# Optimization experiments

Hardware: AMD Instinct MI355X
Metric: run time of the kernel (lower is better)

## Reference

```python
import jax, jax.numpy as jnp
import numpy as np

N, D, E = 16384, 256, 8
H = D // 2  # gate hidden


def setup_inputs() -> dict:
    key = jax.random.key(0)
    ks = jax.random.split(key, 10)
    s = lambda fan_in: 1.0 / np.sqrt(fan_in)
    return {
        "x":   jax.random.normal(ks[0], (N, D), dtype=jnp.float32),
        # gate: Linear(D, D//2) -> ReLU -> Linear(D//2, E) -> Softmax
        "Wg1": jax.random.uniform(ks[1], (D, H), jnp.float32, -s(D), s(D)),
        "bg1": jax.random.uniform(ks[2], (H,), jnp.float32, -s(D), s(D)),
        "Wg2": jax.random.uniform(ks[3], (H, E), jnp.float32, -s(H), s(H)),
        "bg2": jax.random.uniform(ks[4], (E,), jnp.float32, -s(H), s(H)),
        # experts: per-expert Linear(D,D) -> ReLU -> (Dropout eval=identity) -> Linear(D,D)
        "W1": jax.random.uniform(ks[5], (E, D, D), jnp.float32, -s(D), s(D)),
        "b1": jax.random.uniform(ks[6], (E, D), jnp.float32, -s(D), s(D)),
        "W2": jax.random.uniform(ks[7], (E, D, D), jnp.float32, -s(D), s(D)),
        "b2": jax.random.uniform(ks[8], (E, D), jnp.float32, -s(D), s(D)),
    }


def reference(x, Wg1, bg1, Wg2, bg2, W1, b1, W2, b2):
    # gate: [N, E] softmax over experts
    g = jax.nn.softmax(jax.nn.relu(x @ Wg1 + bg1) @ Wg2 + bg2, axis=-1)
    # all experts applied densely via batched GEMMs (fuses the Python loop)
    h = jax.nn.relu(jnp.einsum("nd,edh->neh", x, W1) + b1)  # [N, E, D]
    y = jnp.einsum("neh,ehd->ned", h, W2) + b2              # [N, E, D]
    # weighted combine: sum_e g[n,e] * y[n,e,:]
    return jnp.einsum("ned,ne->nd", y, g)
```

## Files before the change

### kernel.cpp

```cpp
#include <hip/hip_runtime.h>


typedef unsigned short USH;
typedef float f32x4 __attribute__((ext_vector_type(4)));
typedef __bf16 bf16x8 __attribute__((ext_vector_type(8)));

#define AS1 __attribute__((address_space(1)))
#define AS3 __attribute__((address_space(3)))

#define KS 2112

__device__ __forceinline__ USH f2bf(float f) {
  unsigned int u = __float_as_uint(f);
  u += 0x7fffu + ((u >> 16) & 1u);
  return (USH)(u >> 16);
}

__device__ __forceinline__ void gl2lds16(const void* g, void* l) {
  __builtin_amdgcn_global_load_lds((AS1 const void*)g, (AS3 void*)l, 16, 0, 0);
}


__global__ __launch_bounds__(256) void k_prep(
    const float* __restrict__ x,
    const float* __restrict__ Wg1,
    const float* __restrict__ W1,
    const float* __restrict__ W2,  const float* __restrict__ b2,
    USH* __restrict__ xb, USH* __restrict__ wg1t,
    USH* __restrict__ w1t, USH* __restrict__ w2t) {
  __shared__ float T[64][65];
  int b = blockIdx.x, tid = threadIdx.x;

  if (b < 2048) {
    size_t i8 = ((size_t)b * 256 + tid) * 8;
    float4 a = *(const float4*)(x + i8);
    float4 c = *(const float4*)(x + i8 + 4);
    USH v[8];
    v[0] = f2bf(a.x); v[1] = f2bf(a.y); v[2] = f2bf(a.z); v[3] = f2bf(a.w);
    v[4] = f2bf(c.x); v[5] = f2bf(c.y); v[6] = f2bf(c.z); v[7] = f2bf(c.w);
    *(uint4*)(xb + i8) = *(const uint4*)v;
  } else if (b < 2176) {
    int bp = b - 2048;
    int e = bp >> 4, tl = bp & 15;
    int c0 = (tl >> 2) * 64, h0 = (tl & 3) * 64;
    const float* src = W1 + (size_t)e * 65536;
#pragma unroll
    for (int p = 0; p < 4; ++p) {
      int r = p * 16 + (tid >> 4), d4 = (tid & 15) * 4;
      float4 v = *(const float4*)(src + (size_t)(c0 + r) * 256 + h0 + d4);
      T[r][d4] = v.x; T[r][d4 + 1] = v.y; T[r][d4 + 2] = v.z; T[r][d4 + 3] = v.w;
    }
    __syncthreads();
#pragma unroll
    for (int p = 0; p < 4; ++p) {
      int hr = p * 16 + (tid >> 4), c4 = (tid & 15) * 4;
      USH w[4];
#pragma unroll
      for (int j = 0; j < 4; ++j) w[j] = f2bf(T[c4 + j][hr]);
      *(uint2*)(w1t + (size_t)e * 65536 + (size_t)(h0 + hr) * 256 + c0 + c4) = *(const uint2*)w;
    }
  } else if (b < 2184) {
    int bp = b - 2176;
    int c0 = (bp >> 1) * 64, h0 = (bp & 1) * 64;
#pragma unroll
    for (int p = 0; p < 4; ++p) {
      int r = p * 16 + (tid >> 4), d4 = (tid & 15) * 4;
      float4 v = *(const float4*)(Wg1 + (size_t)(c0 + r) * 128 + h0 + d4);
      T[r][d4] = v.x; T[r][d4 + 1] = v.y; T[r][d4 + 2] = v.z; T[r][d4 + 3] = v.w;
    }
    __syncthreads();
#pragma unroll
    for (int p = 0; p < 4; ++p) {
      int hr = p * 16 + (tid >> 4), c4 = (tid & 15) * 4;
      USH w[4];
#pragma unroll
      for (int j = 0; j < 4; ++j) w[j] = f2bf(T[c4 + j][hr]);
      *(uint2*)(wg1t + (size_t)(h0 + hr) * 256 + c0 + c4) = *(const uint2*)w;
    }
  } else if (b < 2312) {
    int bp = b - 2184;
    int e = bp >> 4, tl = bp & 15;
    int h0 = (tl >> 2) * 64, d0 = (tl & 3) * 64;
    const float* src = W2 + (size_t)e * 65536;
#pragma unroll
    for (int p = 0; p < 4; ++p) {
      int r = p * 16 + (tid >> 4), d4 = (tid & 15) * 4;
      float4 v = *(const float4*)(src + (size_t)(h0 + r) * 256 + d0 + d4);
      T[r][d4] = v.x; T[r][d4 + 1] = v.y; T[r][d4 + 2] = v.z; T[r][d4 + 3] = v.w;
    }
    __syncthreads();
#pragma unroll
    for (int p = 0; p < 4; ++p) {
      int dr = p * 16 + (tid >> 4), h4 = (tid & 15) * 4;
      USH w[4];
#pragma unroll
      for (int j = 0; j < 4; ++j) w[j] = f2bf(T[h4 + j][dr]);
      *(uint2*)(w2t + (size_t)(d0 + dr) * KS + e * 256 + h0 + h4) = *(const uint2*)w;
    }
  } else {
    size_t base = (size_t)tid * KS + 2048;
#pragma unroll
    for (int p = 0; p < 16; ++p) {
      USH w[4];
#pragma unroll
      for (int j = 0; j < 4; ++j) {
        int e = p * 4 + j;
        w[j] = (e < 8) ? f2bf(b2[e * 256 + tid]) : (USH)0;
      }
      *(uint2*)(w2t + base + p * 4) = *(const uint2*)w;
    }
  }
}


__global__ __launch_bounds__(256) void k_gate(const USH* __restrict__ xb,
                                              const USH* __restrict__ wg1t,
                                              const float* __restrict__ bg1,
                                              const float* __restrict__ wg2,
                                              const float* __restrict__ bg2,
                                              float* __restrict__ g,
                                              USH* __restrict__ hw) {
  __shared__ __align__(16) USH As[32 * 64];
  __shared__ __align__(16) USH Bs[128 * 64];
  __shared__ float hg[32 * 129];
  __shared__ float bg1s[128];
  __shared__ float w2s[128 * 8];
  __shared__ float b2s[8];
  __shared__ float lg[32 * 8];

  int tid = threadIdx.x;
  int wave = tid >> 6, lane = tid & 63;
  int quad = lane >> 4, l16 = lane & 15;
  int sw = l16 & 7;
  int wr = wave >> 1, wc = wave & 1;
  int rowBase = blockIdx.x * 32;

  for (int t = tid; t < 1024; t += 256) w2s[t] = wg2[t];
  if (tid < 8) b2s[tid] = bg2[tid];
  if (tid < 128) bg1s[tid] = bg1[tid];

  f32x4 acc[4] = {};
  for (int kt = 0; kt < 4; ++kt) {
    int kb = kt * 64;
    {
      int r = tid >> 3, c8 = (tid & 7) ^ (r & 7);
      gl2lds16(xb + (size_t)(rowBase + r) * 256 + kb + c8 * 8, As + (size_t)tid * 8);
    }
#pragma unroll
    for (int c = 0; c < 4; ++c) {
      int i = c * 256 + tid;
      int r = i >> 3, c8 = (i & 7) ^ (r & 7);
      gl2lds16(wg1t + (size_t)r * 256 + kb + c8 * 8, Bs + (size_t)i * 8);
    }
    __syncthreads();
#pragma unroll
    for (int kkc = 0; kkc < 8; kkc += 4) {
      bf16x8 av = *(const bf16x8*)(As + (wr * 16 + l16) * 64 + (((kkc + quad) ^ sw) * 8));
#pragma unroll
      for (int j = 0; j < 4; ++j) {
        bf16x8 bv = *(const bf16x8*)(Bs + (wc * 64 + j * 16 + l16) * 64 + (((kkc + quad) ^ sw) * 8));
        acc[j] = __builtin_amdgcn_mfma_f32_16x16x32_bf16(av, bv, acc[j], 0, 0, 0);
      }
    }
    __syncthreads();
  }

#pragma unroll
  for (int j = 0; j < 4; ++j)
#pragma unroll
    for (int r = 0; r < 4; ++r) {
      int row = wr * 16 + quad * 4 + r;
      int col = wc * 64 + j * 16 + l16;
      hg[row * 129 + col] = fmaxf(acc[j][r] + bg1s[col], 0.0f);
    }
  __syncthreads();

  {
    int row = tid >> 3, p = tid & 7;
    float s = b2s[p];
    for (int k = 0; k < 128; ++k) s += hg[row * 129 + k] * w2s[k * 8 + p];
    lg[row * 8 + p] = s;
  }
  __syncthreads();

  if (tid < 32) {
    float l[8];
    float m = -1e30f;
#pragma unroll
    for (int e = 0; e < 8; ++e) { l[e] = lg[tid * 8 + e]; m = fmaxf(m, l[e]); }
    float s = 0.0f;
#pragma unroll
    for (int e = 0; e < 8; ++e) { l[e] = expf(l[e] - m); s += l[e]; }
    float inv = 1.0f / s;
    size_t grow = rowBase + tid;
#pragma unroll
    for (int e = 0; e < 8; ++e) {
      float ge = l[e] * inv;
      g[grow * 8 + e] = ge;
      hw[grow * KS + 2048 + e] = f2bf(ge);
    }
#pragma unroll
    for (int z = 0; z < 56; ++z) hw[grow * KS + 2056 + z] = 0;
  }
}


__global__ __launch_bounds__(256) void k_stage1(const USH* __restrict__ xb,
                                                const USH* __restrict__ w1t,
                                                const float* __restrict__ b1,
                                                const float* __restrict__ g,
                                                USH* __restrict__ hw) {
  __shared__ __align__(16) USH As[128 * 64];
  __shared__ __align__(16) USH Bs[128 * 64];
  __shared__ float gs[128];
  __shared__ float b1s[128];

  int tid = threadIdx.x;
  int wave = tid >> 6, lane = tid & 63;
  int quad = lane >> 4, l16 = lane & 15;
  int sw = l16 & 7;
  int wr = wave >> 1, wc = wave & 1;
  int rowBase = blockIdx.x * 128;
  int colBase = blockIdx.y * 128;
  int e = blockIdx.z;

  if (tid < 128) {
    gs[tid] = g[(size_t)(rowBase + tid) * 8 + e];
    b1s[tid] = b1[e * 256 + colBase + tid];
  }

  const USH* B = w1t + (size_t)e * 65536;

  f32x4 acc[4][4] = {};
  for (int kt = 0; kt < 4; ++kt) {
    int kb = kt * 64;
#pragma unroll
    for (int c = 0; c < 4; ++c) {
      int i = c * 256 + tid;
      int r = i >> 3, c8 = (i & 7) ^ (r & 7);
      gl2lds16(xb + (size_t)(rowBase + r) * 256 + kb + c8 * 8, As + (size_t)i * 8);
      gl2lds16(B + (size_t)(colBase + r) * 256 + kb + c8 * 8, Bs + (size_t)i * 8);
    }
    __syncthreads();
#pragma unroll
    for (int kkc = 0; kkc < 8; kkc += 4) {
      int cs = ((kkc + quad) ^ sw) * 8;
      bf16x8 av[4], bv[4];
#pragma unroll
      for (int i = 0; i < 4; ++i)
        av[i] = *(const bf16x8*)(As + (wr * 64 + i * 16 + l16) * 64 + cs);
#pragma unroll
      for (int j = 0; j < 4; ++j)
        bv[j] = *(const bf16x8*)(Bs + (wc * 64 + j * 16 + l16) * 64 + cs);
#pragma unroll
      for (int i = 0; i < 4; ++i)
#pragma unroll
        for (int j = 0; j < 4; ++j)
          acc[i][j] = __builtin_amdgcn_mfma_f32_16x16x32_bf16(av[i], bv[j], acc[i][j], 0, 0, 0);
    }
    __syncthreads();
  }

#pragma unroll
  for (int i = 0; i < 4; ++i) {
#pragma unroll
    for (int r = 0; r < 4; ++r) {
      int rl = wr * 64 + i * 16 + quad * 4 + r;
      float gg = gs[rl];
      size_t grow = (size_t)(rowBase + rl);
#pragma unroll
      for (int j = 0; j < 4; ++j) {
        int cl = wc * 64 + j * 16 + l16;
        float v = fmaxf(acc[i][j][r] + b1s[cl], 0.0f) * gg;
        hw[grow * KS + e * 256 + colBase + cl] = f2bf(v);
      }
    }
  }
}


__global__ __launch_bounds__(256) void k_stage2(const USH* __restrict__ hwm,
                                                const USH* __restrict__ w2t,
                                                float* __restrict__ out) {
  __shared__ __align__(16) USH As[64 * 64];
  __shared__ __align__(16) USH Bs[64 * 64];

  int tid = threadIdx.x;
  int wave = tid >> 6, lane = tid & 63;
  int quad = lane >> 4, l16 = lane & 15;
  int sw = l16 & 7;
  int rowBase = blockIdx.x * 64;
  int colBase = blockIdx.y * 64;

  f32x4 acc[4] = {};
  for (int kt = 0; kt < 33; ++kt) {
    int kb = kt * 64;
#pragma unroll
    for (int c = 0; c < 2; ++c) {
      int i = c * 256 + tid;
      int r = i >> 3, c8 = (i & 7) ^ (r & 7);
      gl2lds16(hwm + (size_t)(rowBase + r) * KS + kb + c8 * 8, As + (size_t)i * 8);
      gl2lds16(w2t + (size_t)(colBase + r) * KS + kb + c8 * 8, Bs + (size_t)i * 8);
    }
    __syncthreads();
#pragma unroll
    for (int kkc = 0; kkc < 8; kkc += 4) {
      int cs = ((kkc + quad) ^ sw) * 8;
      bf16x8 av = *(const bf16x8*)(As + (wave * 16 + l16) * 64 + cs);
#pragma unroll
      for (int j = 0; j < 4; ++j) {
        bf16x8 bv = *(const bf16x8*)(Bs + (j * 16 + l16) * 64 + cs);
        acc[j] = __builtin_amdgcn_mfma_f32_16x16x32_bf16(av, bv, acc[j], 0, 0, 0);
      }
    }
    __syncthreads();
  }

#pragma unroll
  for (int j = 0; j < 4; ++j)
#pragma unroll
    for (int r = 0; r < 4; ++r) {
      int row = wave * 16 + quad * 4 + r;
      out[(size_t)(rowBase + row) * 256 + colBase + j * 16 + l16] = acc[j][r];
    }
}


extern "C" void kernel_launch(void* const* d_in, const int* in_sizes, int n_in,
                              void* d_out, int out_size, void* d_ws, size_t ws_size,
                              hipStream_t stream) {
  const float* x   = (const float*)d_in[0];
  const float* Wg1 = (const float*)d_in[1];
  const float* bg1 = (const float*)d_in[2];
  const float* Wg2 = (const float*)d_in[3];
  const float* bg2 = (const float*)d_in[4];
  const float* W1  = (const float*)d_in[5];
  const float* b1  = (const float*)d_in[6];
  const float* W2  = (const float*)d_in[7];
  const float* b2  = (const float*)d_in[8];
  float* out = (float*)d_out;

  char* ws = (char*)d_ws;
  USH*   xb   = (USH*)(ws);
  USH*   w1t  = (USH*)(ws + 8388608);
  USH*   wg1t = (USH*)(ws + 9437184);
  USH*   w2t  = (USH*)(ws + 9502720);
  float* g    = (float*)(ws + 10584064);
  USH*   hw   = (USH*)(ws + 11108352);

  hipLaunchKernelGGL(k_prep, dim3(2313), dim3(256), 0, stream,
                     x, Wg1, W1, W2, b2, xb, wg1t, w1t, w2t);
  hipLaunchKernelGGL(k_gate,   dim3(512),       dim3(256), 0, stream, xb, wg1t, bg1, Wg2, bg2, g, hw);
  hipLaunchKernelGGL(k_stage1, dim3(128, 2, 8), dim3(256), 0, stream, xb, w1t, b1, g, hw);
  hipLaunchKernelGGL(k_stage2, dim3(256, 4),    dim3(256), 0, stream, hw, w2t, out);
}
```

Before: 148.1 us.

## Split-K stage2 into two halves with reduction kernel; stage stage1 epilogue through LDS

Stage2 now runs as a two-way split-K over the 33 K-tiles, writing partial sums to a workspace that a new elementwise kernel adds into the output. This doubles the number of blocks to fill the GPU better. Stage1's epilogue now stages the bf16 results through a swizzled LDS tile and writes them with 16-byte coalesced stores instead of scattered 2-byte stores. The split adds an extra 32 MB round trip of fp32 partials and one more kernel launch.

```diff
diff --git a/kernel.cpp b/kernel.cpp
--- a/kernel.cpp
+++ b/kernel.cpp
@@ -210,10 +210,11 @@
                                                 const float* __restrict__ b1,
                                                 const float* __restrict__ g,
                                                 USH* __restrict__ hw) {
-  __shared__ __align__(16) USH As[128 * 64];
-  __shared__ __align__(16) USH Bs[128 * 64];
+  __shared__ __align__(16) USH smem[128 * 64 * 2];
   __shared__ float gs[128];
   __shared__ float b1s[128];
+  USH* As = smem;
+  USH* Bs = smem + 128 * 64;
 
   int tid = threadIdx.x;
   int wave = tid >> 6, lane = tid & 63;
@@ -267,13 +268,25 @@
     for (int r = 0; r < 4; ++r) {
       int rl = wr * 64 + i * 16 + quad * 4 + r;
       float gg = gs[rl];
-      size_t grow = (size_t)(rowBase + rl);
 #pragma unroll
       for (int j = 0; j < 4; ++j) {
         int cl = wc * 64 + j * 16 + l16;
+        int q = (cl >> 3) ^ (quad << 1);
         float v = fmaxf(acc[i][j][r] + b1s[cl], 0.0f) * gg;
-        hw[grow * KS + e * 256 + colBase + cl] = f2bf(v);
+        smem[rl * 128 + q * 8 + (cl & 7)] = f2bf(v);
       }
+    }
+  }
+  __syncthreads();
+
+  {
+    int rr0 = tid >> 4, qrd = tid & 15;
+#pragma unroll
+    for (int pass = 0; pass < 8; ++pass) {
+      int rr = pass * 16 + rr0;
+      int qp = qrd ^ (((rr >> 2) & 3) << 1);
+      uint4 v = *(const uint4*)(smem + rr * 128 + qp * 8);
+      *(uint4*)(hw + (size_t)(rowBase + rr) * KS + e * 256 + colBase + qrd * 8) = v;
     }
   }
 }
@@ -281,7 +294,7 @@
 
 __global__ __launch_bounds__(256) void k_stage2(const USH* __restrict__ hwm,
                                                 const USH* __restrict__ w2t,
-                                                float* __restrict__ out) {
+                                                float* __restrict__ parts) {
   __shared__ __align__(16) USH As[64 * 64];
   __shared__ __align__(16) USH Bs[64 * 64];
 
@@ -291,9 +304,13 @@
   int sw = l16 & 7;
   int rowBase = blockIdx.x * 64;
   int colBase = blockIdx.y * 64;
+  int z = blockIdx.z;
+  int kt0 = z ? 17 : 0;
+  int kt1 = z ? 33 : 17;
+  float* out = parts + (size_t)z * 16384 * 256;
 
   f32x4 acc[4] = {};
-  for (int kt = 0; kt < 33; ++kt) {
+  for (int kt = kt0; kt < kt1; ++kt) {
     int kb = kt * 64;
 #pragma unroll
     for (int c = 0; c < 2; ++c) {
@@ -323,6 +340,17 @@
       int row = wave * 16 + quad * 4 + r;
       out[(size_t)(rowBase + row) * 256 + colBase + j * 16 + l16] = acc[j][r];
     }
+}
+
+
+__global__ __launch_bounds__(256) void k_add(const float* __restrict__ parts,
+                                             float* __restrict__ out) {
+  size_t i4 = ((size_t)blockIdx.x * 256 + threadIdx.x) * 4;
+  float4 a = *(const float4*)(parts + i4);
+  float4 b = *(const float4*)(parts + 4194304 + i4);
+  float4 o;
+  o.x = a.x + b.x; o.y = a.y + b.y; o.z = a.z + b.z; o.w = a.w + b.w;
+  *(float4*)(out + i4) = o;
 }
 
 
@@ -341,16 +369,18 @@
   float* out = (float*)d_out;
 
   char* ws = (char*)d_ws;
-  USH*   xb   = (USH*)(ws);
-  USH*   w1t  = (USH*)(ws + 8388608);
-  USH*   wg1t = (USH*)(ws + 9437184);
-  USH*   w2t  = (USH*)(ws + 9502720);
-  float* g    = (float*)(ws + 10584064);
-  USH*   hw   = (USH*)(ws + 11108352);
+  USH*   xb    = (USH*)(ws);
+  USH*   w1t   = (USH*)(ws + 8388608);
+  USH*   wg1t  = (USH*)(ws + 9437184);
+  USH*   w2t   = (USH*)(ws + 9502720);
+  float* g     = (float*)(ws + 10584064);
+  USH*   hw    = (USH*)(ws + 11108352);
+  float* parts = (float*)(ws + 80314368);
 
   hipLaunchKernelGGL(k_prep, dim3(2313), dim3(256), 0, stream,
                      x, Wg1, W1, W2, b2, xb, wg1t, w1t, w2t);
   hipLaunchKernelGGL(k_gate,   dim3(512),       dim3(256), 0, stream, xb, wg1t, bg1, Wg2, bg2, g, hw);
   hipLaunchKernelGGL(k_stage1, dim3(128, 2, 8), dim3(256), 0, stream, xb, w1t, b1, g, hw);
-  hipLaunchKernelGGL(k_stage2, dim3(256, 4),    dim3(256), 0, stream, hw, w2t, out);
-}
+  hipLaunchKernelGGL(k_stage2, dim3(256, 4, 2), dim3(256), 0, stream, hw, w2t, parts);
+  hipLaunchKernelGGL(k_add,    dim3(4096),      dim3(256), 0, stream, parts, out);
+}
```

Measured after the change: 162.7 us. 1.1x slower.

## Fuse expert stage1 and stage2 GEMMs into one kernel keeping hidden in LDS

Applied to the files above, without the earlier changes.

Replaces the two expert GEMM kernels and the large gate-weighted hidden buffer in global memory with one kernel. Each block handles 32 rows, loops over the 8 experts, computes the ReLU hidden for each expert into LDS and immediately multiplies it by that expert's W2, adding gate-scaled b2 in registers. This removes the write and re-read of a roughly 70 MB bf16 intermediate and one kernel launch. In exchange it uses only 512 blocks, reloads all expert weights per block, and syncs many times per expert, which may limit occupancy and overlap.

```diff
diff --git a/kernel.cpp b/kernel.cpp
--- a/kernel.cpp
+++ b/kernel.cpp
@@ -7,8 +7,6 @@
 
 #define AS1 __attribute__((address_space(1)))
 #define AS3 __attribute__((address_space(3)))
-
-#define KS 2112
 
 __device__ __forceinline__ USH f2bf(float f) {
   unsigned int u = __float_as_uint(f);
@@ -25,9 +23,9 @@
     const float* __restrict__ x,
     const float* __restrict__ Wg1,
     const float* __restrict__ W1,
-    const float* __restrict__ W2,  const float* __restrict__ b2,
+    const float* __restrict__ W2,
     USH* __restrict__ xb, USH* __restrict__ wg1t,
-    USH* __restrict__ w1t, USH* __restrict__ w2t) {
+    USH* __restrict__ w1t, USH* __restrict__ w2te) {
   __shared__ float T[64][65];
   int b = blockIdx.x, tid = threadIdx.x;
 
@@ -77,7 +75,7 @@
       for (int j = 0; j < 4; ++j) w[j] = f2bf(T[c4 + j][hr]);
       *(uint2*)(wg1t + (size_t)(h0 + hr) * 256 + c0 + c4) = *(const uint2*)w;
     }
-  } else if (b < 2312) {
+  } else {
     int bp = b - 2184;
     int e = bp >> 4, tl = bp & 15;
     int h0 = (tl >> 2) * 64, d0 = (tl & 3) * 64;
@@ -95,19 +93,7 @@
       USH w[4];
 #pragma unroll
       for (int j = 0; j < 4; ++j) w[j] = f2bf(T[h4 + j][dr]);
-      *(uint2*)(w2t + (size_t)(d0 + dr) * KS + e * 256 + h0 + h4) = *(const uint2*)w;
-    }
-  } else {
-    size_t base = (size_t)tid * KS + 2048;
-#pragma unroll
-    for (int p = 0; p < 16; ++p) {
-      USH w[4];
-#pragma unroll
-      for (int j = 0; j < 4; ++j) {
-        int e = p * 4 + j;
-        w[j] = (e < 8) ? f2bf(b2[e * 256 + tid]) : (USH)0;
-      }
-      *(uint2*)(w2t + base + p * 4) = *(const uint2*)w;
+      *(uint2*)(w2te + (size_t)e * 65536 + (size_t)(d0 + dr) * 256 + h0 + h4) = *(const uint2*)w;
     }
   }
 }
@@ -118,8 +104,7 @@
                                               const float* __restrict__ bg1,
                                               const float* __restrict__ wg2,
                                               const float* __restrict__ bg2,
-                                              float* __restrict__ g,
-                                              USH* __restrict__ hw) {
+                                              float* __restrict__ g) {
   __shared__ __align__(16) USH As[32 * 64];
   __shared__ __align__(16) USH Bs[128 * 64];
   __shared__ float hg[32 * 129];
@@ -194,134 +179,133 @@
     float inv = 1.0f / s;
     size_t grow = rowBase + tid;
 #pragma unroll
-    for (int e = 0; e < 8; ++e) {
-      float ge = l[e] * inv;
-      g[grow * 8 + e] = ge;
-      hw[grow * KS + 2048 + e] = f2bf(ge);
-    }
-#pragma unroll
-    for (int z = 0; z < 56; ++z) hw[grow * KS + 2056 + z] = 0;
-  }
-}
-
-
-__global__ __launch_bounds__(256) void k_stage1(const USH* __restrict__ xb,
-                                                const USH* __restrict__ w1t,
-                                                const float* __restrict__ b1,
-                                                const float* __restrict__ g,
-                                                USH* __restrict__ hw) {
-  __shared__ __align__(16) USH As[128 * 64];
-  __shared__ __align__(16) USH Bs[128 * 64];
-  __shared__ float gs[128];
-  __shared__ float b1s[128];
+    for (int e = 0; e < 8; ++e) g[grow * 8 + e] = l[e] * inv;
+  }
+}
+
+
+__global__ __launch_bounds__(256) void k_experts(const USH* __restrict__ xb,
+                                                 const USH* __restrict__ w1t,
+                                                 const USH* __restrict__ w2te,
+                                                 const float* __restrict__ g,
+                                                 const float* __restrict__ b1,
+                                                 const float* __restrict__ b2,
+                                                 float* __restrict__ out) {
+  __shared__ __align__(16) USH Xs[32 * 256];
+  __shared__ __align__(16) USH Hs[32 * 256];
+  __shared__ __align__(16) USH Bs[256 * 64];
+  __shared__ float gs[32];
 
   int tid = threadIdx.x;
   int wave = tid >> 6, lane = tid & 63;
   int quad = lane >> 4, l16 = lane & 15;
   int sw = l16 & 7;
-  int wr = wave >> 1, wc = wave & 1;
-  int rowBase = blockIdx.x * 128;
-  int colBase = blockIdx.y * 128;
-  int e = blockIdx.z;
-
-  if (tid < 128) {
-    gs[tid] = g[(size_t)(rowBase + tid) * 8 + e];
-    b1s[tid] = b1[e * 256 + colBase + tid];
-  }
-
-  const USH* B = w1t + (size_t)e * 65536;
-
-  f32x4 acc[4][4] = {};
-  for (int kt = 0; kt < 4; ++kt) {
-    int kb = kt * 64;
-#pragma unroll
-    for (int c = 0; c < 4; ++c) {
-      int i = c * 256 + tid;
-      int r = i >> 3, c8 = (i & 7) ^ (r & 7);
-      gl2lds16(xb + (size_t)(rowBase + r) * 256 + kb + c8 * 8, As + (size_t)i * 8);
-      gl2lds16(B + (size_t)(colBase + r) * 256 + kb + c8 * 8, Bs + (size_t)i * 8);
-    }
-    __syncthreads();
-#pragma unroll
-    for (int kkc = 0; kkc < 8; kkc += 4) {
-      int cs = ((kkc + quad) ^ sw) * 8;
-      bf16x8 av[4], bv[4];
-#pragma unroll
-      for (int i = 0; i < 4; ++i)
-        av[i] = *(const bf16x8*)(As + (wr * 64 + i * 16 + l16) * 64 + cs);
-#pragma unroll
-      for (int j = 0; j < 4; ++j)
-        bv[j] = *(const bf16x8*)(Bs + (wc * 64 + j * 16 + l16) * 64 + cs);
-#pragma unroll
-      for (int i = 0; i < 4; ++i)
-#pragma unroll
-        for (int j = 0; j < 4; ++j)
-          acc[i][j] = __builtin_amdgcn_mfma_f32_16x16x32_bf16(av[i], bv[j], acc[i][j], 0, 0, 0);
-    }
-    __syncthreads();
-  }
-
-#pragma unroll
-  for (int i = 0; i < 4; ++i) {
-#pragma unroll
-    for (int r = 0; r < 4; ++r) {
-      int rl = wr * 64 + i * 16 + quad * 4 + r;
-      float gg = gs[rl];
-      size_t grow = (size_t)(rowBase + rl);
-#pragma unroll
-      for (int j = 0; j < 4; ++j) {
-        int cl = wc * 64 + j * 16 + l16;
-        float v = fmaxf(acc[i][j][r] + b1s[cl], 0.0f) * gg;
-        hw[grow * KS + e * 256 + colBase + cl] = f2bf(v);
-      }
-    }
-  }
-}
-
-
-__global__ __launch_bounds__(256) void k_stage2(const USH* __restrict__ hwm,
-                                                const USH* __restrict__ w2t,
-                                                float* __restrict__ out) {
-  __shared__ __align__(16) USH As[64 * 64];
-  __shared__ __align__(16) USH Bs[64 * 64];
-
-  int tid = threadIdx.x;
-  int wave = tid >> 6, lane = tid & 63;
-  int quad = lane >> 4, l16 = lane & 15;
-  int sw = l16 & 7;
-  int rowBase = blockIdx.x * 64;
-  int colBase = blockIdx.y * 64;
-
-  f32x4 acc[4] = {};
-  for (int kt = 0; kt < 33; ++kt) {
-    int kb = kt * 64;
-#pragma unroll
-    for (int c = 0; c < 2; ++c) {
-      int i = c * 256 + tid;
-      int r = i >> 3, c8 = (i & 7) ^ (r & 7);
-      gl2lds16(hwm + (size_t)(rowBase + r) * KS + kb + c8 * 8, As + (size_t)i * 8);
-      gl2lds16(w2t + (size_t)(colBase + r) * KS + kb + c8 * 8, Bs + (size_t)i * 8);
-    }
-    __syncthreads();
-#pragma unroll
-    for (int kkc = 0; kkc < 8; kkc += 4) {
-      int cs = ((kkc + quad) ^ sw) * 8;
-      bf16x8 av = *(const bf16x8*)(As + (wave * 16 + l16) * 64 + cs);
-#pragma unroll
-      for (int j = 0; j < 4; ++j) {
-        bf16x8 bv = *(const bf16x8*)(Bs + (j * 16 + l16) * 64 + cs);
-        acc[j] = __builtin_amdgcn_mfma_f32_16x16x32_bf16(av, bv, acc[j], 0, 0, 0);
-      }
-    }
-    __syncthreads();
-  }
-
-#pragma unroll
-  for (int j = 0; j < 4; ++j)
-#pragma unroll
-    for (int r = 0; r < 4; ++r) {
-      int row = wave * 16 + quad * 4 + r;
-      out[(size_t)(rowBase + row) * 256 + colBase + j * 16 + l16] = acc[j][r];
+  int rowBase = blockIdx.x * 32;
+
+#pragma unroll
+  for (int p = 0; p < 4; ++p) {
+    int i = p * 256 + tid;
+    int r = i >> 5, c = (i & 31) ^ (r & 7);
+    gl2lds16(xb + (size_t)(rowBase + r) * 256 + c * 8, Xs + (size_t)i * 8);
+  }
+
+  f32x4 acc_out[2][4] = {};
+
+  for (int e = 0; e < 8; ++e) {
+    __syncthreads();
+    if (tid < 32) gs[tid] = g[(size_t)(rowBase + tid) * 8 + e];
+    const USH* W1e = w1t + (size_t)e * 65536;
+    const USH* W2e = w2te + (size_t)e * 65536;
+
+    f32x4 acc_h[2][4] = {};
+    for (int kt = 0; kt < 4; ++kt) {
+#pragma unroll
+      for (int p = 0; p < 8; ++p) {
+        int i = p * 256 + tid;
+        int r = i >> 3, c = (i & 7) ^ (r & 7);
+        gl2lds16(W1e + (size_t)r * 256 + kt * 64 + c * 8, Bs + (size_t)i * 8);
+      }
+      __syncthreads();
+#pragma unroll
+      for (int kh = 0; kh < 2; ++kh) {
+        int w = kt * 2 + kh;
+        bf16x8 av[2], bv[4];
+#pragma unroll
+        for (int rt = 0; rt < 2; ++rt)
+          av[rt] = *(const bf16x8*)(Xs + ((rt * 16 + l16) * 32 + ((w * 4 + quad) ^ sw)) * 8);
+#pragma unroll
+        for (int ct = 0; ct < 4; ++ct)
+          bv[ct] = *(const bf16x8*)(Bs + ((wave * 64 + ct * 16 + l16) * 8 + ((kh * 4 + quad) ^ sw)) * 8);
+#pragma unroll
+        for (int rt = 0; rt < 2; ++rt)
+#pragma unroll
+          for (int ct = 0; ct < 4; ++ct)
+            acc_h[rt][ct] = __builtin_amdgcn_mfma_f32_16x16x32_bf16(av[rt], bv[ct], acc_h[rt][ct], 0, 0, 0);
+      }
+      __syncthreads();
+    }
+
+#pragma unroll
+    for (int rt = 0; rt < 2; ++rt)
+#pragma unroll
+      for (int rr = 0; rr < 4; ++rr) {
+        int hr = rt * 16 + quad * 4 + rr;
+        float gg = gs[hr];
+#pragma unroll
+        for (int ct = 0; ct < 4; ++ct) {
+          int col = wave * 64 + ct * 16 + l16;
+          float v = fmaxf(acc_h[rt][ct][rr] + b1[e * 256 + col], 0.0f) * gg;
+          Hs[hr * 256 + (((col >> 3) ^ (hr & 7)) * 8) + (col & 7)] = f2bf(v);
+        }
+      }
+    __syncthreads();
+
+    for (int kt = 0; kt < 4; ++kt) {
+#pragma unroll
+      for (int p = 0; p < 8; ++p) {
+        int i = p * 256 + tid;
+        int r = i >> 3, c = (i & 7) ^ (r & 7);
+        gl2lds16(W2e + (size_t)r * 256 + kt * 64 + c * 8, Bs + (size_t)i * 8);
+      }
+      __syncthreads();
+#pragma unroll
+      for (int kh = 0; kh < 2; ++kh) {
+        int w = kt * 2 + kh;
+        bf16x8 av[2], bv[4];
+#pragma unroll
+        for (int rt = 0; rt < 2; ++rt)
+          av[rt] = *(const bf16x8*)(Hs + ((rt * 16 + l16) * 32 + ((w * 4 + quad) ^ sw)) * 8);
+#pragma unroll
+        for (int ct = 0; ct < 4; ++ct)
+          bv[ct] = *(const bf16x8*)(Bs + ((wave * 64 + ct * 16 + l16) * 8 + ((kh * 4 + quad) ^ sw)) * 8);
+#pragma unroll
+        for (int rt = 0; rt < 2; ++rt)
+#pragma unroll
+          for (int ct = 0; ct < 4; ++ct)
+            acc_out[rt][ct] = __builtin_amdgcn_mfma_f32_16x16x32_bf16(av[rt], bv[ct], acc_out[rt][ct], 0, 0, 0);
+      }
+      __syncthreads();
+    }
+
+#pragma unroll
+    for (int ct = 0; ct < 4; ++ct) {
+      float b2c = b2[e * 256 + wave * 64 + ct * 16 + l16];
+#pragma unroll
+      for (int rt = 0; rt < 2; ++rt)
+#pragma unroll
+        for (int rr = 0; rr < 4; ++rr)
+          acc_out[rt][ct][rr] += gs[rt * 16 + quad * 4 + rr] * b2c;
+    }
+  }
+
+#pragma unroll
+  for (int rt = 0; rt < 2; ++rt)
+#pragma unroll
+    for (int rr = 0; rr < 4; ++rr) {
+      size_t grow = (size_t)(rowBase + rt * 16 + quad * 4 + rr);
+#pragma unroll
+      for (int ct = 0; ct < 4; ++ct)
+        out[grow * 256 + wave * 64 + ct * 16 + l16] = acc_out[rt][ct][rr];
     }
 }
 
@@ -341,16 +325,14 @@
   float* out = (float*)d_out;
 
   char* ws = (char*)d_ws;
-  USH*   xb   = (USH*)(ws);
-  USH*   w1t  = (USH*)(ws + 8388608);
-  USH*   wg1t = (USH*)(ws + 9437184);
-  USH*   w2t  = (USH*)(ws + 9502720);
-  float* g    = (float*)(ws + 10584064);
-  USH*   hw   = (USH*)(ws + 11108352);
-
-  hipLaunchKernelGGL(k_prep, dim3(2313), dim3(256), 0, stream,
-                     x, Wg1, W1, W2, b2, xb, wg1t, w1t, w2t);
-  hipLaunchKernelGGL(k_gate,   dim3(512),       dim3(256), 0, stream, xb, wg1t, bg1, Wg2, bg2, g, hw);
-  hipLaunchKernelGGL(k_stage1, dim3(128, 2, 8), dim3(256), 0, stream, xb, w1t, b1, g, hw);
-  hipLaunchKernelGGL(k_stage2, dim3(256, 4),    dim3(256), 0, stream, hw, w2t, out);
-}
+  USH*   xb    = (USH*)(ws);
+  USH*   w1t   = (USH*)(ws + 8388608);
+  USH*   wg1t  = (USH*)(ws + 9437184);
+  USH*   w2te  = (USH*)(ws + 9502720);
+  float* g     = (float*)(ws + 10551296);
+
+  hipLaunchKernelGGL(k_prep, dim3(2312), dim3(256), 0, stream,
+                     x, Wg1, W1, W2, xb, wg1t, w1t, w2te);
+  hipLaunchKernelGGL(k_gate,    dim3(512), dim3(256), 0, stream, xb, wg1t, bg1, Wg2, bg2, g);
+  hipLaunchKernelGGL(k_experts, dim3(512), dim3(256), 0, stream, xb, w1t, w2te, g, b1, b2, out);
+}
```

After: 156.5 us. +5.7%, slower.
